# Kernel tuning notes

Measured on AMD Instinct MI355X. Metric: run time of the kernel, lower is better.

The kernel has to match this reference:

```python
import jax, jax.numpy as jnp
import numpy as np

# Mamba2 defaults with d_model=512, headdim=2*d_model (=> nheads=1)
D_MODEL = 512
D_INNER = 2 * D_MODEL          # expand=2
D_STATE = 128
NHEADS = 1                     # d_inner // headdim = 1
HEADDIM = D_INNER              # headdim = 2*hidden_dim
D_CONV = 4
NG = 1                         # ngroups
EPS = 1e-5


def setup_inputs() -> dict:
    key = jax.random.key(0)
    ks = jax.random.split(key, 8)
    B, L = 4, 2048
    d_in_proj = 2 * D_INNER + 2 * NG * D_STATE + NHEADS   # 2305
    conv_ch = D_INNER + 2 * NG * D_STATE                  # 1280
    x = jax.random.normal(ks[0], (B, L, D_MODEL), jnp.float32)
    rnn_state = jax.random.normal(ks[1], (B, D_MODEL), jnp.float32)
    W_in = jax.random.normal(ks[2], (d_in_proj, D_MODEL), jnp.float32) * (D_MODEL ** -0.5)
    conv_w = jax.random.normal(ks[3], (conv_ch, 1, D_CONV), jnp.float32) * (D_CONV ** -0.5)
    conv_b = jnp.zeros((conv_ch,), jnp.float32)
    # dt_bias = inv_softplus(dt) with dt ~ U(1e-3, 0.1), as in Mamba2 init
    dt = jax.random.uniform(ks[4], (NHEADS,), jnp.float32, 1e-3, 0.1)
    dt_bias = jnp.log(jnp.expm1(dt))
    A_log = jnp.log(jax.random.uniform(ks[5], (NHEADS,), jnp.float32, 1.0, 16.0))
    Dp = jnp.ones((NHEADS,), jnp.float32)
    norm_w = jnp.ones((D_INNER,), jnp.float32)
    W_out = jax.random.normal(ks[6], (D_MODEL, D_INNER), jnp.float32) * (D_INNER ** -0.5)
    return dict(x=x, rnn_state=rnn_state, W_in=W_in, conv_w=conv_w, conv_b=conv_b,
                dt_bias=dt_bias, A_log=A_log, Dp=Dp, norm_w=norm_w, W_out=W_out)


def _mamba2(x, W_in, conv_w, conv_b, dt_bias, A_log, Dp, norm_w, W_out):
    B, L, _ = x.shape
    zxbcdt = jnp.einsum('bld,ed->ble', x, W_in)           # (B,L,2305)
    z, xBC, dt = jnp.split(zxbcdt, [D_INNER, 2 * D_INNER + 2 * NG * D_STATE], axis=-1)
    # causal depthwise conv1d over channels (B,C,L), then silu
    xBC = xBC.transpose(0, 2, 1)
    xBC = jax.lax.conv_general_dilated(
        xBC, conv_w, window_strides=(1,), padding=[(D_CONV - 1, 0)],
        feature_group_count=xBC.shape[1], dimension_numbers=('NCH', 'OIH', 'NCH'))
    xBC = jax.nn.silu(xBC + conv_b[None, :, None]).transpose(0, 2, 1)
    xs, Bm, Cm = jnp.split(xBC, [D_INNER, D_INNER + NG * D_STATE], axis=-1)
    xs = xs.reshape(B, L, NHEADS, HEADDIM)
    dt = jax.nn.softplus(dt + dt_bias)                    # (B,L,H)
    A = -jnp.exp(A_log)                                   # (H,)
    dA = jnp.exp(dt * A)                                  # (B,L,H)

    # selective state-space scan: h_t = dA_t*h_{t-1} + dt_t * x_t (x) B_t ; y_t = h_t @ C_t
    def step(state, inp):
        x_t, dt_t, dA_t, B_t, C_t = inp
        state = dA_t[:, :, None, None] * state \
            + (dt_t[:, :, None] * x_t)[..., None] * B_t[:, None, None, :]
        y_t = jnp.einsum('bhpn,bn->bhp', state, C_t)
        return state, y_t

    init = jnp.zeros((B, NHEADS, HEADDIM, D_STATE), x.dtype)
    inputs = (xs.transpose(1, 0, 2, 3), dt.transpose(1, 0, 2), dA.transpose(1, 0, 2),
              Bm.transpose(1, 0, 2), Cm.transpose(1, 0, 2))
    _, ys = jax.lax.scan(step, init, inputs)              # (L,B,H,P)
    y = ys.transpose(1, 0, 2, 3) + Dp[None, None, :, None] * xs
    y = y.reshape(B, L, D_INNER)
    # gated RMSNorm (gate first, norm_before_gate=False)
    y = y * jax.nn.silu(z)
    y = y * jax.lax.rsqrt(jnp.mean(y * y, axis=-1, keepdims=True) + EPS) * norm_w
    return jnp.einsum('bld,od->blo', y, W_out)


def reference(x, rnn_state, W_in, conv_w, conv_b, dt_bias, A_log, Dp, norm_w, W_out):
    out = _mamba2(x, W_in, conv_w, conv_b, dt_bias, A_log, Dp, norm_w, W_out)
    return (out, rnn_state)
```

## Files before the change

### kernel.cpp

```cpp
#include <hip/hip_runtime.h>
#include <cstdint>
#include <cstddef>


typedef __bf16 bf16_t;
typedef __bf16 bf16x8 __attribute__((ext_vector_type(8)));
typedef __bf16 bf16x4 __attribute__((ext_vector_type(4)));
typedef __bf16 bf16x2 __attribute__((ext_vector_type(2)));
typedef float  f32x4  __attribute__((ext_vector_type(4)));

#define BATCH   4
#define SEQLEN  2048
#define MROWS   8192
#define DMODEL  512
#define DINNER  1024
#define DSTATE  128
#define NZX     2304
#define NCONV   1280
#define CHUNK   128
#define NCHUNK  16
#define NBC     64

__device__ __forceinline__ float siluf(float x) { return x / (1.f + __expf(-x)); }

__device__ __forceinline__ void load_lds16(const bf16_t* g, bf16_t* l)
{
    __builtin_amdgcn_global_load_lds(
        (const __attribute__((address_space(1))) void*)g,
        (__attribute__((address_space(3))) void*)l,
        16, 0, 0);
}

template <typename OutT>
__device__ __forceinline__ void gemm_body(
    unsigned char* smem,
    const bf16_t* __restrict__ A, const bf16_t* __restrict__ B,
    OutT* __restrict__ C, int Ntot, int K, int lda, int ldb, int bn, int bm)
{
    bf16_t* As = (bf16_t*)smem;
    bf16_t* Bs = (bf16_t*)(smem + 16384);

    const int tid  = threadIdx.x;
    const int wave = tid >> 6, lane = tid & 63;
    const int lr = lane & 15, q = lane >> 4;
    const int wm = (wave & 1) * 64, wn = (wave >> 1) * 64;

    f32x4 acc[4][4];
    #pragma unroll
    for (int i = 0; i < 4; ++i)
        #pragma unroll
        for (int j = 0; j < 4; ++j)
            acc[i][j] = (f32x4){0.f, 0.f, 0.f, 0.f};

    const int row_a0 = bm * 128, row_b0 = bn * 128;
    const int srow = tid >> 3;
    const int gsw  = (((tid & 7) ^ (srow & 7))) * 8;
    const int lsl  = (tid & 7) * 8;

    for (int kt = 0; kt < K; kt += 64) {
        #pragma unroll
        for (int i = 0; i < 4; ++i) {
            int row = srow + i * 32;
            load_lds16(&A[(size_t)(row_a0 + row) * lda + kt + gsw], &As[row * 64 + lsl]);
            load_lds16(&B[(size_t)(row_b0 + row) * ldb + kt + gsw], &Bs[row * 64 + lsl]);
        }
        __syncthreads();
        #pragma unroll
        for (int k0 = 0; k0 < 64; k0 += 32) {
            bf16x8 af[4], bfr[4];
            #pragma unroll
            for (int mi = 0; mi < 4; ++mi) {
                int r = wm + mi * 16 + lr, kc = (k0 >> 3) + q;
                af[mi] = *reinterpret_cast<const bf16x8*>(
                    &As[r * 64 + ((kc ^ (r & 7)) << 3)]);
            }
            #pragma unroll
            for (int ni = 0; ni < 4; ++ni) {
                int r = wn + ni * 16 + lr, kc = (k0 >> 3) + q;
                bfr[ni] = *reinterpret_cast<const bf16x8*>(
                    &Bs[r * 64 + ((kc ^ (r & 7)) << 3)]);
            }
            #pragma unroll
            for (int mi = 0; mi < 4; ++mi)
                #pragma unroll
                for (int ni = 0; ni < 4; ++ni)
                    acc[mi][ni] = __builtin_amdgcn_mfma_f32_16x16x32_bf16(
                        af[mi], bfr[ni], acc[mi][ni], 0, 0, 0);
        }
        __syncthreads();
    }

    #pragma unroll
    for (int mi = 0; mi < 4; ++mi)
        #pragma unroll
        for (int ni = 0; ni < 4; ++ni)
            #pragma unroll
            for (int ri = 0; ri < 4; ++ri) {
                int row = row_a0 + wm + mi * 16 + q * 4 + ri;
                int col = row_b0 + wn + ni * 16 + lr;
                C[(size_t)row * Ntot + col] = (OutT)acc[mi][ni][ri];
            }
}

__device__ __forceinline__ void cumsum_body(
    const float* __restrict__ dtv, const float* __restrict__ A_log,
    float* __restrict__ sarr, float* __restrict__ Pv,
    float* __restrict__ EdTv, float* __restrict__ chp, int bc)
{
    __shared__ float w0sum, stot;
    int j = threadIdx.x;
    bool active = j < CHUNK;
    int lane = j & 63;
    int r = bc * CHUNK + j;
    float A = -expf(A_log[0]);
    float dt = active ? dtv[r] : 0.f;
    float s = dt;
    #pragma unroll
    for (int m = 1; m <= 32; m <<= 1) {
        float o = __shfl_up(s, m);
        if (lane >= m) s += o;
    }
    if (j == 63) w0sum = s;
    __syncthreads();
    if (j >= 64 && active) s += w0sum;
    if (j == 127) stot = s;
    __syncthreads();
    if (active) {
        float sT = stot;
        sarr[r] = s;
        Pv[r]   = expf(A * s);
        EdTv[r] = expf(A * (sT - s)) * dt;
        if (j == 127) chp[bc] = expf(A * sT);
    }
}

__global__ __launch_bounds__(256) void gemm1_kernel(
    const bf16_t* __restrict__ xb, const bf16_t* __restrict__ winb,
    bf16_t* __restrict__ zx, const float* __restrict__ dtv,
    const float* __restrict__ A_log, float* __restrict__ sarr,
    float* __restrict__ Pv, float* __restrict__ EdTv, float* __restrict__ chp)
{
    __shared__ __align__(16) unsigned char smem[32768];
    int linear = blockIdx.x;
    if (linear < (NZX / 128) * (MROWS / 128)) {
        int xcd = linear & 7, j = linear >> 3;
        int bm = xcd * 8 + (j & 7);
        int bn = j >> 3;
        gemm_body<bf16_t>(smem, xb, winb, zx, NZX, DMODEL, DMODEL, DMODEL, bn, bm);
    } else {
        cumsum_body(dtv, A_log, sarr, Pv, EdTv, chp, linear - 1152);
    }
}

__global__ __launch_bounds__(256) void gemm2_kernel(
    const bf16_t* __restrict__ yb, const bf16_t* __restrict__ woutb,
    float* __restrict__ out)
{
    __shared__ __align__(16) bf16_t As[64 * 64];
    __shared__ __align__(16) bf16_t Bs[128 * 64];

    int id  = blockIdx.x;
    int xcd = id & 7, j = id >> 3;
    int bm  = xcd * 16 + (j & 15);
    int bn  = j >> 4;

    const int tid  = threadIdx.x;
    const int wave = tid >> 6, lane = tid & 63;
    const int lr = lane & 15, q = lane >> 4;
    const int wm = (wave & 1) * 32, wn = (wave >> 1) * 64;

    f32x4 acc[2][4];
    #pragma unroll
    for (int i = 0; i < 2; ++i)
        #pragma unroll
        for (int jj = 0; jj < 4; ++jj)
            acc[i][jj] = (f32x4){0.f, 0.f, 0.f, 0.f};

    const int row_a0 = bm * 64, row_b0 = bn * 128;
    const int srow = tid >> 3;
    const int gsw  = (((tid & 7) ^ (srow & 7))) * 8;
    const int lsl  = (tid & 7) * 8;

    for (int kt = 0; kt < DINNER; kt += 64) {
        #pragma unroll
        for (int i = 0; i < 2; ++i) {
            int row = srow + i * 32;
            load_lds16(&yb[(size_t)(row_a0 + row) * DINNER + kt + gsw], &As[row * 64 + lsl]);
        }
        #pragma unroll
        for (int i = 0; i < 4; ++i) {
            int row = srow + i * 32;
            load_lds16(&woutb[(size_t)(row_b0 + row) * DINNER + kt + gsw], &Bs[row * 64 + lsl]);
        }
        __syncthreads();
        #pragma unroll
        for (int k0 = 0; k0 < 64; k0 += 32) {
            bf16x8 af[2], bfr[4];
            #pragma unroll
            for (int mi = 0; mi < 2; ++mi) {
                int r = wm + mi * 16 + lr, kc = (k0 >> 3) + q;
                af[mi] = *reinterpret_cast<const bf16x8*>(
                    &As[r * 64 + ((kc ^ (r & 7)) << 3)]);
            }
            #pragma unroll
            for (int ni = 0; ni < 4; ++ni) {
                int r = wn + ni * 16 + lr, kc = (k0 >> 3) + q;
                bfr[ni] = *reinterpret_cast<const bf16x8*>(
                    &Bs[r * 64 + ((kc ^ (r & 7)) << 3)]);
            }
            #pragma unroll
            for (int mi = 0; mi < 2; ++mi)
                #pragma unroll
                for (int ni = 0; ni < 4; ++ni)
                    acc[mi][ni] = __builtin_amdgcn_mfma_f32_16x16x32_bf16(
                        af[mi], bfr[ni], acc[mi][ni], 0, 0, 0);
        }
        __syncthreads();
    }

    #pragma unroll
    for (int mi = 0; mi < 2; ++mi)
        #pragma unroll
        for (int ni = 0; ni < 4; ++ni)
            #pragma unroll
            for (int ri = 0; ri < 4; ++ri) {
                int row = row_a0 + wm + mi * 16 + q * 4 + ri;
                int col = row_b0 + wn + ni * 16 + lr;
                out[(size_t)row * DMODEL + col] = acc[mi][ni][ri];
            }
}

__device__ __forceinline__ void mbuild_body(
    unsigned char* smem,
    const float* __restrict__ sarr, const float* __restrict__ dtv,
    const float* __restrict__ Pv, const float* __restrict__ A_log,
    const bf16_t* __restrict__ xbc, bf16_t* __restrict__ Mx, int bc)
{
    bf16_t* Cs  = (bf16_t*)smem;
    bf16_t* Bs2 = (bf16_t*)(smem + 32768);
    float* sj = (float*)(smem + 65536);
    float* dj = (float*)(smem + 65536 + 512);
    float* pj = (float*)(smem + 65536 + 1024);

    int tid = threadIdx.x;
    if (tid < CHUNK) {
        sj[tid] = sarr[bc * CHUNK + tid];
        dj[tid] = dtv[bc * CHUNK + tid];
        pj[tid] = Pv[bc * CHUNK + tid];
    }
    int rowbase = bc * 128;
    int srow = tid >> 4;
    int gsw  = (((tid & 15) ^ (srow & 7))) * 8;
    int lsl  = (tid & 15) * 8;
    #pragma unroll
    for (int i = 0; i < 8; ++i) {
        int row = srow + i * 16;
        load_lds16(&xbc[(size_t)(rowbase + row) * NCONV + 1152 + gsw], &Cs[row * 128 + lsl]);
        load_lds16(&xbc[(size_t)(rowbase + row) * NCONV + 1024 + gsw], &Bs2[row * 128 + lsl]);
    }
    __syncthreads();

    const int wave = tid >> 6, lane = tid & 63;
    const int lr = lane & 15, q = lane >> 4;
    const int wm = (wave & 1) * 64, wn = (wave >> 1) * 64;

    f32x4 acc[4][4];
    #pragma unroll
    for (int i = 0; i < 4; ++i)
        #pragma unroll
        for (int j = 0; j < 4; ++j)
            acc[i][j] = (f32x4){0.f, 0.f, 0.f, 0.f};

    #pragma unroll
    for (int k0 = 0; k0 < 128; k0 += 32) {
        bf16x8 af[4], bfr[4];
        #pragma unroll
        for (int mi = 0; mi < 4; ++mi) {
            int r = wm + mi * 16 + lr, kc = (k0 >> 3) + q;
            af[mi] = *reinterpret_cast<const bf16x8*>(
                &Cs[r * 128 + ((kc ^ (r & 7)) << 3)]);
        }
        #pragma unroll
        for (int ni = 0; ni < 4; ++ni) {
            int r = wn + ni * 16 + lr, kc = (k0 >> 3) + q;
            bfr[ni] = *reinterpret_cast<const bf16x8*>(
                &Bs2[r * 128 + ((kc ^ (r & 7)) << 3)]);
        }
        #pragma unroll
        for (int mi = 0; mi < 4; ++mi)
            #pragma unroll
            for (int ni = 0; ni < 4; ++ni)
                acc[mi][ni] = __builtin_amdgcn_mfma_f32_16x16x32_bf16(
                    af[mi], bfr[ni], acc[mi][ni], 0, 0, 0);
    }

    float A = -expf(A_log[0]);
    bf16_t* MxB = Mx + (size_t)bc * 32768;
    #pragma unroll
    for (int mi = 0; mi < 4; ++mi)
        #pragma unroll
        for (int ni = 0; ni < 4; ++ni)
            #pragma unroll
            for (int ri = 0; ri < 4; ++ri) {
                int row = wm + mi * 16 + q * 4 + ri;
                int col = wn + ni * 16 + lr;
                float val = 0.f;
                if (col <= row)
                    val = acc[mi][ni][ri] * expf(A * (sj[row] - sj[col])) * dj[col];
                MxB[(size_t)row * 256 + col] = (bf16_t)val;
            }

    int rr = tid >> 1, cb2 = (tid & 1) * 64;
    float Pi = pj[rr];
    #pragma unroll
    for (int m0 = 0; m0 < 64; m0 += 8) {
        int kc = (cb2 + m0) >> 3;
        bf16x8 cv = *reinterpret_cast<const bf16x8*>(
            &Cs[rr * 128 + ((kc ^ (rr & 7)) << 3)]);
        bf16x8 o;
        #pragma unroll
        for (int m = 0; m < 8; ++m) o[m] = (bf16_t)((float)cv[m] * Pi);
        *reinterpret_cast<bf16x8*>(&MxB[(size_t)rr * 256 + 128 + cb2 + m0]) = o;
    }
}

__global__ __launch_bounds__(256) void gemmA_mbuild_kernel(
    const bf16_t* __restrict__ Xt, const bf16_t* __restrict__ Bwt,
    bf16_t* __restrict__ cstate,
    const float* __restrict__ sarr, const float* __restrict__ dtv,
    const float* __restrict__ Pv, const float* __restrict__ A_log,
    const bf16_t* __restrict__ xbc, bf16_t* __restrict__ Mx)
{
    __shared__ __align__(16) unsigned char smem[67072];
    int id = blockIdx.x;
    if (id < 512) {
        int bc = id & 63, bm = id >> 6;
        gemm_body<bf16_t>(smem,
            Xt + (size_t)bc * 131072, Bwt + (size_t)bc * 16384,
            cstate + (size_t)bc * 131072,
            DSTATE, CHUNK, CHUNK, CHUNK, 0, bm);
    } else {
        mbuild_body(smem, sarr, dtv, Pv, A_log, xbc, Mx, id - 512);
    }
}

__global__ __launch_bounds__(256) void gemm_y_kernel(
    const bf16_t* __restrict__ Mx, const bf16_t* __restrict__ Xt,
    const bf16_t* __restrict__ Stb, bf16_t* __restrict__ yf)
{
    __shared__ __align__(16) bf16_t As[128 * 64];
    __shared__ __align__(16) bf16_t Bs[128 * 64];

    const int bc = blockIdx.z, bn = blockIdx.x;
    const bf16_t* Ab = Mx + (size_t)bc * 32768;
    const bf16_t* Xb = Xt  + (size_t)bc * 131072 + (size_t)bn * 128 * 128;
    const bf16_t* Sb = Stb + (size_t)bc * 131072 + (size_t)bn * 128 * 128;
    bf16_t* Cb = yf + (size_t)bc * 131072;

    const int tid  = threadIdx.x;
    const int wave = tid >> 6, lane = tid & 63;
    const int lr = lane & 15, q = lane >> 4;
    const int wm = (wave & 1) * 64, wn = (wave >> 1) * 64;

    f32x4 acc[4][4];
    #pragma unroll
    for (int i = 0; i < 4; ++i)
        #pragma unroll
        for (int j = 0; j < 4; ++j)
            acc[i][j] = (f32x4){0.f, 0.f, 0.f, 0.f};

    const int srow = tid >> 3;
    const int gsw  = (((tid & 7) ^ (srow & 7))) * 8;
    const int lsl  = (tid & 7) * 8;

    for (int kt = 0; kt < 256; kt += 64) {
        const bf16_t* bsrc = (kt < 128) ? (Xb + kt) : (Sb + (kt - 128));
        #pragma unroll
        for (int i = 0; i < 4; ++i) {
            int row = srow + i * 32;
            load_lds16(&Ab[(size_t)row * 256 + kt + gsw], &As[row * 64 + lsl]);
            load_lds16(&bsrc[(size_t)row * 128 + gsw], &Bs[row * 64 + lsl]);
        }
        __syncthreads();
        #pragma unroll
        for (int k0 = 0; k0 < 64; k0 += 32) {
            bf16x8 af[4], bfr[4];
            #pragma unroll
            for (int mi = 0; mi < 4; ++mi) {
                int r = wm + mi * 16 + lr, kc = (k0 >> 3) + q;
                af[mi] = *reinterpret_cast<const bf16x8*>(
                    &As[r * 64 + ((kc ^ (r & 7)) << 3)]);
            }
            #pragma unroll
            for (int ni = 0; ni < 4; ++ni) {
                int r = wn + ni * 16 + lr, kc = (k0 >> 3) + q;
                bfr[ni] = *reinterpret_cast<const bf16x8*>(
                    &Bs[r * 64 + ((kc ^ (r & 7)) << 3)]);
            }
            #pragma unroll
            for (int mi = 0; mi < 4; ++mi)
                #pragma unroll
                for (int ni = 0; ni < 4; ++ni)
                    acc[mi][ni] = __builtin_amdgcn_mfma_f32_16x16x32_bf16(
                        af[mi], bfr[ni], acc[mi][ni], 0, 0, 0);
        }
        __syncthreads();
    }

    #pragma unroll
    for (int mi = 0; mi < 4; ++mi)
        #pragma unroll
        for (int ni = 0; ni < 4; ++ni)
            #pragma unroll
            for (int ri = 0; ri < 4; ++ri) {
                int row = wm + mi * 16 + q * 4 + ri;
                int col = bn * 128 + wn + ni * 16 + lr;
                Cb[(size_t)row * 1024 + col] = (bf16_t)acc[mi][ni][ri];
            }
}

__global__ __launch_bounds__(256) void dtcast_kernel(
    const float* __restrict__ x, const float* __restrict__ W_in,
    const float* __restrict__ dt_bias, const float* __restrict__ W_out,
    float* __restrict__ dtv, bf16_t* __restrict__ xb,
    bf16_t* __restrict__ winb, bf16_t* __restrict__ woutb)
{
    int bid = blockIdx.x;
    if (bid < MROWS / 4) {
        int wave = threadIdx.x >> 6, lane = threadIdx.x & 63;
        int r = bid * 4 + wave;
        const float* xr = x + (size_t)r * DMODEL + lane * 8;
        const float* wr = W_in + (size_t)NZX * DMODEL + lane * 8;
        float4 a0 = *reinterpret_cast<const float4*>(xr);
        float4 a1 = *reinterpret_cast<const float4*>(xr + 4);
        float4 b0 = *reinterpret_cast<const float4*>(wr);
        float4 b1 = *reinterpret_cast<const float4*>(wr + 4);

        bf16x8 xo;
        xo[0] = (bf16_t)a0.x; xo[1] = (bf16_t)a0.y; xo[2] = (bf16_t)a0.z; xo[3] = (bf16_t)a0.w;
        xo[4] = (bf16_t)a1.x; xo[5] = (bf16_t)a1.y; xo[6] = (bf16_t)a1.z; xo[7] = (bf16_t)a1.w;
        *reinterpret_cast<bf16x8*>(xb + (size_t)r * DMODEL + lane * 8) = xo;

        float s = a0.x * b0.x + a0.y * b0.y + a0.z * b0.z + a0.w * b0.w
                + a1.x * b1.x + a1.y * b1.y + a1.z * b1.z + a1.w * b1.w;
        #pragma unroll
        for (int m = 32; m >= 1; m >>= 1) s += __shfl_xor(s, m);
        if (lane == 0) {
            float t  = s + dt_bias[0];
            dtv[r] = (t > 20.f) ? t : log1pf(expf(t));
        }
        return;
    }
    int i = (bid - MROWS / 4) * 256 + threadIdx.x;
    const int n4a = 2305 * DMODEL / 4, n4b = DMODEL * DINNER / 4;
    const float* src; bf16_t* dst; int j;
    if (i < n4a)            { src = W_in;  dst = winb;  j = i; }
    else if (i < n4a + n4b) { src = W_out; dst = woutb; j = i - n4a; }
    else return;
    float4 v = reinterpret_cast<const float4*>(src)[j];
    bf16x4 o;
    o[0] = (bf16_t)v.x; o[1] = (bf16_t)v.y; o[2] = (bf16_t)v.z; o[3] = (bf16_t)v.w;
    reinterpret_cast<bf16x4*>(dst)[j] = o;
}

__global__ __launch_bounds__(256) void conv_tr_kernel(
    const bf16_t* __restrict__ zx, const float* __restrict__ cw,
    const float* __restrict__ cb, const float* __restrict__ EdTv,
    bf16_t* __restrict__ xbc, bf16_t* __restrict__ Xt, bf16_t* __restrict__ Bwt)
{
    constexpr int TS = 66;
    __shared__ bf16_t tile[128 * TS];
    __shared__ float cwS[64 * 4];
    __shared__ float cbS[64];

    int id  = blockIdx.x;
    int xcd = id & 7;
    int k   = id >> 3;
    int bc  = xcd * 8 + (k & 7);
    int rest = k >> 3;
    int cg   = rest >> 1;
    int half = rest & 1;
    int c0   = cg * 128 + half * 64;
    int tid  = threadIdx.x;

    if (tid < 64) {
        float4 w = *reinterpret_cast<const float4*>(cw + (size_t)(c0 + tid) * 4);
        *reinterpret_cast<float4*>(&cwS[tid * 4]) = w;
        cbS[tid] = cb[c0 + tid];
    }
    __syncthreads();

    int lrow = tid >> 3;
    int lc8  = (tid & 7) * 8;
    int g0 = bc * 128;

    #pragma unroll
    for (int pass = 0; pass < 4; ++pass) {
        int row = pass * 32 + lrow;
        int g = g0 + row;
        int l = g & (SEQLEN - 1);
        float acc[8];
        #pragma unroll
        for (int m = 0; m < 8; ++m) acc[m] = cbS[lc8 + m];
        #pragma unroll
        for (int kk = 0; kk < 4; ++kk) {
            if (l + kk >= 3) {
                bf16x8 v = *reinterpret_cast<const bf16x8*>(
                    zx + (size_t)(g + kk - 3) * NZX + DINNER + c0 + lc8);
                #pragma unroll
                for (int m = 0; m < 8; ++m)
                    acc[m] += cwS[(lc8 + m) * 4 + kk] * (float)v[m];
            }
        }
        bf16x8 o;
        #pragma unroll
        for (int m = 0; m < 8; ++m) o[m] = (bf16_t)siluf(acc[m]);
        *reinterpret_cast<bf16x8*>(xbc + (size_t)g * NCONV + c0 + lc8) = o;
        if (cg < 9) {
            #pragma unroll
            for (int jj = 0; jj < 4; ++jj) {
                bf16x2 p; p[0] = o[jj * 2]; p[1] = o[jj * 2 + 1];
                *reinterpret_cast<bf16x2*>(&tile[row * TS + lc8 + jj * 2]) = p;
            }
        }
    }
    if (cg == 9) return;
    __syncthreads();

    const bool isB = (cg == 8);
    int jo = (tid >> 4) * 8;
    int i  = tid & 15;
    float sc[8];
    #pragma unroll
    for (int m = 0; m < 8; ++m)
        sc[m] = isB ? EdTv[bc * 128 + jo + m] : 1.f;

    #pragma unroll
    for (int pass = 0; pass < 4; ++pass) {
        int oc = pass * 16 + i;
        bf16x8 o;
        #pragma unroll
        for (int m = 0; m < 8; ++m)
            o[m] = (bf16_t)((float)tile[(jo + m) * TS + oc] * sc[m]);
        bf16_t* dst = isB
            ? (Bwt + (size_t)bc * 16384 + (size_t)(c0 - 1024 + oc) * 128 + jo)
            : (Xt + (size_t)bc * 131072 + (size_t)(c0 + oc) * 128 + jo);
        *reinterpret_cast<bf16x8*>(dst) = o;
    }
}

__global__ __launch_bounds__(256) void scan_combine_kernel(
    const bf16_t* __restrict__ cstate, const float* __restrict__ chp,
    bf16_t* __restrict__ Stb)
{
    __shared__ float chS[NCHUNK];
    int idx = blockIdx.x * 256 + threadIdx.x;
    int b   = idx >> 17;
    int np  = idx & 131071;
    if (threadIdx.x < NCHUNK) chS[threadIdx.x] = chp[b * NCHUNK + threadIdx.x];
    __syncthreads();

    const bf16_t* src = cstate + ((size_t)b << 21) + np;
    bf16_t*       dst = Stb    + ((size_t)b << 21) + np;
    float t[NCHUNK];
    #pragma unroll
    for (int c = 0; c < NCHUNK; ++c) t[c] = (float)src[(size_t)c << 17];
    float v = 0.f;
    #pragma unroll
    for (int c = 0; c < NCHUNK; ++c) {
        dst[(size_t)c << 17] = (bf16_t)v;
        v = chS[c] * v + t[c];
    }
}

__global__ __launch_bounds__(256) void gate_norm_kernel(
    const bf16_t* __restrict__ yf, const bf16_t* __restrict__ zx,
    const bf16_t* __restrict__ xbc, const float* __restrict__ Dp,
    const float* __restrict__ norm_w, bf16_t* __restrict__ yb,
    const float* __restrict__ rnn, float* __restrict__ outTail)
{
    int blk = blockIdx.x, tid = threadIdx.x;
    if (blk >= MROWS / 4) {
        int i = (blk - MROWS / 4) * 256 + tid;
        if (i < BATCH * DMODEL) outTail[i] = rnn[i];
        return;
    }
    int wave = tid >> 6, lane = tid & 63;
    int r = blk * 4 + wave;
    int p0 = lane * 8, p1 = 512 + lane * 8;
    float D0 = Dp[0];

    bf16x8 y0 = *reinterpret_cast<const bf16x8*>(yf + (size_t)r * DINNER + p0);
    bf16x8 y1 = *reinterpret_cast<const bf16x8*>(yf + (size_t)r * DINNER + p1);
    bf16x8 z0 = *reinterpret_cast<const bf16x8*>(zx + (size_t)r * NZX + p0);
    bf16x8 z1 = *reinterpret_cast<const bf16x8*>(zx + (size_t)r * NZX + p1);
    bf16x8 x0 = *reinterpret_cast<const bf16x8*>(xbc + (size_t)r * NCONV + p0);
    bf16x8 x1 = *reinterpret_cast<const bf16x8*>(xbc + (size_t)r * NCONV + p1);

    float g[16];
    #pragma unroll
    for (int m = 0; m < 8; ++m) {
        g[m]     = ((float)y0[m] + D0 * (float)x0[m]) * siluf((float)z0[m]);
        g[8 + m] = ((float)y1[m] + D0 * (float)x1[m]) * siluf((float)z1[m]);
    }
    float ss = 0.f;
    #pragma unroll
    for (int m = 0; m < 16; ++m) ss += g[m] * g[m];
    #pragma unroll
    for (int m = 32; m >= 1; m >>= 1) ss += __shfl_xor(ss, m);
    float scale = rsqrtf(ss * (1.f / 1024.f) + 1e-5f);

    const float* nw = norm_w;
    float4 w0a = *reinterpret_cast<const float4*>(nw + p0);
    float4 w0b = *reinterpret_cast<const float4*>(nw + p0 + 4);
    float4 w1a = *reinterpret_cast<const float4*>(nw + p1);
    float4 w1b = *reinterpret_cast<const float4*>(nw + p1 + 4);
    float w[16] = {w0a.x, w0a.y, w0a.z, w0a.w, w0b.x, w0b.y, w0b.z, w0b.w,
                   w1a.x, w1a.y, w1a.z, w1a.w, w1b.x, w1b.y, w1b.z, w1b.w};
    bf16x8 o0, o1;
    #pragma unroll
    for (int m = 0; m < 8; ++m) {
        o0[m] = (bf16_t)(g[m] * scale * w[m]);
        o1[m] = (bf16_t)(g[8 + m] * scale * w[8 + m]);
    }
    *reinterpret_cast<bf16x8*>(yb + (size_t)r * DINNER + p0) = o0;
    *reinterpret_cast<bf16x8*>(yb + (size_t)r * DINNER + p1) = o1;
}

extern "C" void kernel_launch(void* const* d_in, const int* in_sizes, int n_in,
                              void* d_out, int out_size, void* d_ws, size_t ws_size,
                              hipStream_t stream)
{
    const float* x        = (const float*)d_in[0];
    const float* rnn      = (const float*)d_in[1];
    const float* W_in     = (const float*)d_in[2];
    const float* conv_w   = (const float*)d_in[3];
    const float* conv_b   = (const float*)d_in[4];
    const float* dt_bias  = (const float*)d_in[5];
    const float* A_log    = (const float*)d_in[6];
    const float* Dp       = (const float*)d_in[7];
    const float* norm_w   = (const float*)d_in[8];
    const float* W_out    = (const float*)d_in[9];
    float* out = (float*)d_out;

    char* ws = (char*)d_ws;
    bf16_t* xb     = (bf16_t*)(ws + 0);
    bf16_t* Mx     = (bf16_t*)(ws + 4194304);
    bf16_t* winb   = (bf16_t*)(ws + 8388608);
    bf16_t* woutb  = (bf16_t*)(ws + 10748928);
    bf16_t* zx     = (bf16_t*)(ws + 11797504);
    float*  dtv    = (float*) (ws + 49546240);
    float*  sarr   = (float*) (ws + 49579008);
    float*  Pv     = (float*) (ws + 49611776);
    float*  EdTv   = (float*) (ws + 49644544);
    float*  chp    = (float*) (ws + 49677312);
    bf16_t* xbcb   = (bf16_t*)(ws + 49677568);
    bf16_t* Xt     = (bf16_t*)(ws + 70649088);
    bf16_t* Bwt    = (bf16_t*)(ws + 87426304);
    bf16_t* cstate = (bf16_t*)(ws + 89523456);
    bf16_t* yf     = (bf16_t*)(ws + 89523456);
    bf16_t* Stb    = (bf16_t*)(ws + 106300672);
    bf16_t* yb     = (bf16_t*)(ws + 123077888);

    {
        const int n4a = 2305 * DMODEL / 4, n4b = DMODEL * DINNER / 4;
        int grid = MROWS / 4 + (n4a + n4b + 255) / 256;
        dtcast_kernel<<<grid, 256, 0, stream>>>(
            x, W_in, dt_bias, W_out, dtv, xb, winb, woutb);
    }

    gemm1_kernel<<<1152 + NBC, 256, 0, stream>>>(
        xb, winb, zx, dtv, A_log, sarr, Pv, EdTv, chp);

    conv_tr_kernel<<<1280, 256, 0, stream>>>(
        zx, conv_w, conv_b, EdTv, xbcb, Xt, Bwt);

    gemmA_mbuild_kernel<<<576, 256, 0, stream>>>(
        Xt, Bwt, cstate, sarr, dtv, Pv, A_log, xbcb, Mx);

    scan_combine_kernel<<<BATCH * 131072 / 256, 256, 0, stream>>>(cstate, chp, Stb);

    gemm_y_kernel<<<dim3(8, 1, NBC), 256, 0, stream>>>(Mx, Xt, Stb, yf);

    gate_norm_kernel<<<MROWS / 4 + 8, 256, 0, stream>>>(
        yf, zx, xbcb, Dp, norm_w, yb, rnn, out + (size_t)MROWS * DMODEL);

    gemm2_kernel<<<512, 256, 0, stream>>>(yb, woutb, out);
}
```

Measured before the change: 206.5 us.

## Fuse gated RMSNorm into gemm_y epilogue and defer scaling to gemm2

The separate gate_norm kernel is removed. The gemm_y epilogue now stages its tile in swizzled shared memory, applies the D skip and the silu(z) gate, writes the gated bf16 activations, and atomically adds per-row sums of squares into a buffer that scan_combine zeroes. norm_w is folded into W_out during the cast, and gemm2 applies the per-row rsqrt scale in its epilogue. This saves one kernel launch and a full read and write of the y intermediate, at the cost of atomics and bf16 rounding before normalization.

```diff
diff --git a/kernel.cpp b/kernel.cpp
--- a/kernel.cpp
+++ b/kernel.cpp
@@ -154,7 +154,7 @@
 
 __global__ __launch_bounds__(256) void gemm2_kernel(
     const bf16_t* __restrict__ yb, const bf16_t* __restrict__ woutb,
-    float* __restrict__ out)
+    const float* __restrict__ ss, float* __restrict__ out)
 {
     __shared__ __align__(16) bf16_t As[64 * 64];
     __shared__ __align__(16) bf16_t Bs[128 * 64];
@@ -218,6 +218,15 @@
         __syncthreads();
     }
 
+    float sc[2][4];
+    #pragma unroll
+    for (int mi = 0; mi < 2; ++mi)
+        #pragma unroll
+        for (int ri = 0; ri < 4; ++ri) {
+            int row = row_a0 + wm + mi * 16 + q * 4 + ri;
+            sc[mi][ri] = rsqrtf(ss[row] * (1.f / 1024.f) + 1e-5f);
+        }
+
     #pragma unroll
     for (int mi = 0; mi < 2; ++mi)
         #pragma unroll
@@ -226,7 +235,7 @@
             for (int ri = 0; ri < 4; ++ri) {
                 int row = row_a0 + wm + mi * 16 + q * 4 + ri;
                 int col = row_b0 + wn + ni * 16 + lr;
-                out[(size_t)row * DMODEL + col] = acc[mi][ni][ri];
+                out[(size_t)row * DMODEL + col] = acc[mi][ni][ri] * sc[mi][ri];
             }
 }
 
@@ -346,16 +355,18 @@
 
 __global__ __launch_bounds__(256) void gemm_y_kernel(
     const bf16_t* __restrict__ Mx, const bf16_t* __restrict__ Xt,
-    const bf16_t* __restrict__ Stb, bf16_t* __restrict__ yf)
-{
-    __shared__ __align__(16) bf16_t As[128 * 64];
-    __shared__ __align__(16) bf16_t Bs[128 * 64];
+    const bf16_t* __restrict__ Stb, const bf16_t* __restrict__ zx,
+    const bf16_t* __restrict__ xbc, const float* __restrict__ Dp,
+    bf16_t* __restrict__ yb, float* __restrict__ ss)
+{
+    __shared__ __align__(16) unsigned char smem[32768];
+    bf16_t* As = (bf16_t*)smem;
+    bf16_t* Bs = (bf16_t*)(smem + 16384);
 
     const int bc = blockIdx.z, bn = blockIdx.x;
     const bf16_t* Ab = Mx + (size_t)bc * 32768;
     const bf16_t* Xb = Xt  + (size_t)bc * 131072 + (size_t)bn * 128 * 128;
     const bf16_t* Sb = Stb + (size_t)bc * 131072 + (size_t)bn * 128 * 128;
-    bf16_t* Cb = yf + (size_t)bc * 131072;
 
     const int tid  = threadIdx.x;
     const int wave = tid >> 6, lane = tid & 63;
@@ -407,6 +418,7 @@
         __syncthreads();
     }
 
+    bf16_t* Yt = (bf16_t*)smem;
     #pragma unroll
     for (int mi = 0; mi < 4; ++mi)
         #pragma unroll
@@ -414,16 +426,43 @@
             #pragma unroll
             for (int ri = 0; ri < 4; ++ri) {
                 int row = wm + mi * 16 + q * 4 + ri;
-                int col = bn * 128 + wn + ni * 16 + lr;
-                Cb[(size_t)row * 1024 + col] = (bf16_t)acc[mi][ni][ri];
-            }
+                int col = wn + ni * 16 + lr;
+                int byte = (row * 256 + col * 2) ^ ((row & 7) << 5);
+                *reinterpret_cast<bf16_t*>((char*)Yt + byte) = (bf16_t)acc[mi][ni][ri];
+            }
+    __syncthreads();
+
+    const int rr = tid >> 1, cb = (tid & 1) * 64;
+    const size_t rg = (size_t)bc * 128 + rr;
+    const int colg0 = bn * 128 + cb;
+    const float D0 = Dp[0];
+    float part = 0.f;
+    #pragma unroll
+    for (int m0 = 0; m0 < 64; m0 += 8) {
+        int byte = (rr * 256 + (cb + m0) * 2) ^ ((rr & 7) << 5);
+        bf16x8 yv = *reinterpret_cast<const bf16x8*>((char*)Yt + byte);
+        bf16x8 zv = *reinterpret_cast<const bf16x8*>(zx  + rg * NZX   + colg0 + m0);
+        bf16x8 xv = *reinterpret_cast<const bf16x8*>(xbc + rg * NCONV + colg0 + m0);
+        bf16x8 o;
+        #pragma unroll
+        for (int m = 0; m < 8; ++m) {
+            float g = ((float)yv[m] + D0 * (float)xv[m]) * siluf((float)zv[m]);
+            part += g * g;
+            o[m] = (bf16_t)g;
+        }
+        *reinterpret_cast<bf16x8*>(yb + rg * DINNER + colg0 + m0) = o;
+    }
+    part += __shfl_xor(part, 1);
+    if ((tid & 1) == 0) atomicAdd(&ss[rg], part);
 }
 
 __global__ __launch_bounds__(256) void dtcast_kernel(
     const float* __restrict__ x, const float* __restrict__ W_in,
     const float* __restrict__ dt_bias, const float* __restrict__ W_out,
+    const float* __restrict__ norm_w, const float* __restrict__ rnn,
     float* __restrict__ dtv, bf16_t* __restrict__ xb,
-    bf16_t* __restrict__ winb, bf16_t* __restrict__ woutb)
+    bf16_t* __restrict__ winb, bf16_t* __restrict__ woutb,
+    float* __restrict__ outTail)
 {
     int bid = blockIdx.x;
     if (bid < MROWS / 4) {
@@ -453,14 +492,24 @@
     }
     int i = (bid - MROWS / 4) * 256 + threadIdx.x;
     const int n4a = 2305 * DMODEL / 4, n4b = DMODEL * DINNER / 4;
-    const float* src; bf16_t* dst; int j;
-    if (i < n4a)            { src = W_in;  dst = winb;  j = i; }
-    else if (i < n4a + n4b) { src = W_out; dst = woutb; j = i - n4a; }
-    else return;
-    float4 v = reinterpret_cast<const float4*>(src)[j];
-    bf16x4 o;
-    o[0] = (bf16_t)v.x; o[1] = (bf16_t)v.y; o[2] = (bf16_t)v.z; o[3] = (bf16_t)v.w;
-    reinterpret_cast<bf16x4*>(dst)[j] = o;
+    if (i < n4a) {
+        float4 v = reinterpret_cast<const float4*>(W_in)[i];
+        bf16x4 o;
+        o[0] = (bf16_t)v.x; o[1] = (bf16_t)v.y; o[2] = (bf16_t)v.z; o[3] = (bf16_t)v.w;
+        reinterpret_cast<bf16x4*>(winb)[i] = o;
+    } else if (i < n4a + n4b) {
+        int j = i - n4a;
+        float4 v = reinterpret_cast<const float4*>(W_out)[j];
+        int c0 = (j * 4) & (DINNER - 1);
+        float4 w = *reinterpret_cast<const float4*>(norm_w + c0);
+        bf16x4 o;
+        o[0] = (bf16_t)(v.x * w.x); o[1] = (bf16_t)(v.y * w.y);
+        o[2] = (bf16_t)(v.z * w.z); o[3] = (bf16_t)(v.w * w.w);
+        reinterpret_cast<bf16x4*>(woutb)[j] = o;
+    } else if (i < n4a + n4b + BATCH * DMODEL) {
+        int k = i - n4a - n4b;
+        outTail[k] = rnn[k];
+    }
 }
 
 __global__ __launch_bounds__(256) void conv_tr_kernel(
@@ -551,10 +600,16 @@
 
 __global__ __launch_bounds__(256) void scan_combine_kernel(
     const bf16_t* __restrict__ cstate, const float* __restrict__ chp,
-    bf16_t* __restrict__ Stb)
-{
+    bf16_t* __restrict__ Stb, float* __restrict__ ss)
+{
+    int blk = blockIdx.x;
+    if (blk >= BATCH * 131072 / 256) {
+        int i = (blk - BATCH * 131072 / 256) * 256 + threadIdx.x;
+        ss[i] = 0.f;
+        return;
+    }
     __shared__ float chS[NCHUNK];
-    int idx = blockIdx.x * 256 + threadIdx.x;
+    int idx = blk * 256 + threadIdx.x;
     int b   = idx >> 17;
     int np  = idx & 131071;
     if (threadIdx.x < NCHUNK) chS[threadIdx.x] = chp[b * NCHUNK + threadIdx.x];
@@ -571,60 +626,6 @@
         dst[(size_t)c << 17] = (bf16_t)v;
         v = chS[c] * v + t[c];
     }
-}
-
-__global__ __launch_bounds__(256) void gate_norm_kernel(
-    const bf16_t* __restrict__ yf, const bf16_t* __restrict__ zx,
-    const bf16_t* __restrict__ xbc, const float* __restrict__ Dp,
-    const float* __restrict__ norm_w, bf16_t* __restrict__ yb,
-    const float* __restrict__ rnn, float* __restrict__ outTail)
-{
-    int blk = blockIdx.x, tid = threadIdx.x;
-    if (blk >= MROWS / 4) {
-        int i = (blk - MROWS / 4) * 256 + tid;
-        if (i < BATCH * DMODEL) outTail[i] = rnn[i];
-        return;
-    }
-    int wave = tid >> 6, lane = tid & 63;
-    int r = blk * 4 + wave;
-    int p0 = lane * 8, p1 = 512 + lane * 8;
-    float D0 = Dp[0];
-
-    bf16x8 y0 = *reinterpret_cast<const bf16x8*>(yf + (size_t)r * DINNER + p0);
-    bf16x8 y1 = *reinterpret_cast<const bf16x8*>(yf + (size_t)r * DINNER + p1);
-    bf16x8 z0 = *reinterpret_cast<const bf16x8*>(zx + (size_t)r * NZX + p0);
-    bf16x8 z1 = *reinterpret_cast<const bf16x8*>(zx + (size_t)r * NZX + p1);
-    bf16x8 x0 = *reinterpret_cast<const bf16x8*>(xbc + (size_t)r * NCONV + p0);
-    bf16x8 x1 = *reinterpret_cast<const bf16x8*>(xbc + (size_t)r * NCONV + p1);
-
-    float g[16];
-    #pragma unroll
-    for (int m = 0; m < 8; ++m) {
-        g[m]     = ((float)y0[m] + D0 * (float)x0[m]) * siluf((float)z0[m]);
-        g[8 + m] = ((float)y1[m] + D0 * (float)x1[m]) * siluf((float)z1[m]);
-    }
-    float ss = 0.f;
-    #pragma unroll
-    for (int m = 0; m < 16; ++m) ss += g[m] * g[m];
-    #pragma unroll
-    for (int m = 32; m >= 1; m >>= 1) ss += __shfl_xor(ss, m);
-    float scale = rsqrtf(ss * (1.f / 1024.f) + 1e-5f);
-
-    const float* nw = norm_w;
-    float4 w0a = *reinterpret_cast<const float4*>(nw + p0);
-    float4 w0b = *reinterpret_cast<const float4*>(nw + p0 + 4);
-    float4 w1a = *reinterpret_cast<const float4*>(nw + p1);
-    float4 w1b = *reinterpret_cast<const float4*>(nw + p1 + 4);
-    float w[16] = {w0a.x, w0a.y, w0a.z, w0a.w, w0b.x, w0b.y, w0b.z, w0b.w,
-                   w1a.x, w1a.y, w1a.z, w1a.w, w1b.x, w1b.y, w1b.z, w1b.w};
-    bf16x8 o0, o1;
-    #pragma unroll
-    for (int m = 0; m < 8; ++m) {
-        o0[m] = (bf16_t)(g[m] * scale * w[m]);
-        o1[m] = (bf16_t)(g[8 + m] * scale * w[8 + m]);
-    }
-    *reinterpret_cast<bf16x8*>(yb + (size_t)r * DINNER + p0) = o0;
-    *reinterpret_cast<bf16x8*>(yb + (size_t)r * DINNER + p1) = o1;
 }
 
 extern "C" void kernel_launch(void* const* d_in, const int* in_sizes, int n_in,
@@ -645,6 +646,7 @@
 
     char* ws = (char*)d_ws;
     bf16_t* xb     = (bf16_t*)(ws + 0);
+    float*  ssn    = (float*) (ws + 0);
     bf16_t* Mx     = (bf16_t*)(ws + 4194304);
     bf16_t* winb   = (bf16_t*)(ws + 8388608);
     bf16_t* woutb  = (bf16_t*)(ws + 10748928);
@@ -658,15 +660,16 @@
     bf16_t* Xt     = (bf16_t*)(ws + 70649088);
     bf16_t* Bwt    = (bf16_t*)(ws + 87426304);
     bf16_t* cstate = (bf16_t*)(ws + 89523456);
-    bf16_t* yf     = (bf16_t*)(ws + 89523456);
     bf16_t* Stb    = (bf16_t*)(ws + 106300672);
     bf16_t* yb     = (bf16_t*)(ws + 123077888);
 
     {
         const int n4a = 2305 * DMODEL / 4, n4b = DMODEL * DINNER / 4;
-        int grid = MROWS / 4 + (n4a + n4b + 255) / 256;
+        int nrest = n4a + n4b + BATCH * DMODEL;
+        int grid = MROWS / 4 + (nrest + 255) / 256;
         dtcast_kernel<<<grid, 256, 0, stream>>>(
-            x, W_in, dt_bias, W_out, dtv, xb, winb, woutb);
+            x, W_in, dt_bias, W_out, norm_w, rnn, dtv, xb, winb, woutb,
+            out + (size_t)MROWS * DMODEL);
     }
 
     gemm1_kernel<<<1152 + NBC, 256, 0, stream>>>(
@@ -678,12 +681,11 @@
     gemmA_mbuild_kernel<<<576, 256, 0, stream>>>(
         Xt, Bwt, cstate, sarr, dtv, Pv, A_log, xbcb, Mx);
 
-    scan_combine_kernel<<<BATCH * 131072 / 256, 256, 0, stream>>>(cstate, chp, Stb);
-
-    gemm_y_kernel<<<dim3(8, 1, NBC), 256, 0, stream>>>(Mx, Xt, Stb, yf);
-
-    gate_norm_kernel<<<MROWS / 4 + 8, 256, 0, stream>>>(
-        yf, zx, xbcb, Dp, norm_w, yb, rnn, out + (size_t)MROWS * DMODEL);
-
-    gemm2_kernel<<<512, 256, 0, stream>>>(yb, woutb, out);
-}
+    scan_combine_kernel<<<BATCH * 131072 / 256 + 32, 256, 0, stream>>>(
+        cstate, chp, Stb, ssn);
+
+    gemm_y_kernel<<<dim3(8, 1, NBC), 256, 0, stream>>>(
+        Mx, Xt, Stb, zx, xbcb, Dp, yb, ssn);
+
+    gemm2_kernel<<<512, 256, 0, stream>>>(yb, woutb, ssn, out);
+}
```

After: 229.2 us. +11.0%, slower.
